# Optimization experiments

Measured on AMD Instinct MI355X. Metric: run time of the kernel, lower is better.

The kernel has to match this reference:

```python
import jax, jax.numpy as jnp
import numpy as np

EPS = 1e-12

def _layer_norm(x, g, b):
    mu = jnp.mean(x, axis=-1, keepdims=True)
    var = jnp.mean(jnp.square(x - mu), axis=-1, keepdims=True)
    return (x - mu) * jax.lax.rsqrt(var + EPS) * g + b

def setup_inputs() -> dict:
    key = jax.random.key(0)
    ks = jax.random.split(key, 16)
    B, S, D, H, F = 2, 2048, 1024, 16, 4096
    s = 0.02
    inp = {
        "x": jax.random.normal(ks[0], (B, S, D), jnp.float32),
        "Wq": jax.random.normal(ks[1], (D, D), jnp.float32) * s,
        "bq": jnp.zeros((D,), jnp.float32),
        "Wk": jax.random.normal(ks[2], (D, D), jnp.float32) * s,
        "bk": jnp.zeros((D,), jnp.float32),
        "Wv": jax.random.normal(ks[3], (D, D), jnp.float32) * s,
        "bv": jnp.zeros((D,), jnp.float32),
        "Wo": jax.random.normal(ks[4], (D, D), jnp.float32) * s,
        "bo": jnp.zeros((D,), jnp.float32),
        "ln1_g": jnp.ones((D,), jnp.float32),
        "ln1_b": jnp.zeros((D,), jnp.float32),
        "W1": jax.random.normal(ks[5], (D, F), jnp.float32) * s,
        "b1": jnp.zeros((F,), jnp.float32),
        "W2": jax.random.normal(ks[6], (F, D), jnp.float32) * s,
        "b2": jnp.zeros((D,), jnp.float32),
        "ln2_g": jnp.ones((D,), jnp.float32),
        "ln2_b": jnp.zeros((D,), jnp.float32),
    }
    return inp

def reference(x, Wq, bq, Wk, bk, Wv, bv, Wo, bo, ln1_g, ln1_b, W1, b1, W2, b2, ln2_g, ln2_b):
    B, S, D = x.shape
    H = 16
    hd = D // H
    # q/k/v projections -> (B, H, S, hd)
    def split_heads(t):
        return t.reshape(B, S, H, hd).transpose(0, 2, 1, 3)
    q = split_heads(x @ Wq + bq)
    k = split_heads(x @ Wk + bk)
    v = split_heads(x @ Wv + bv)
    # naive attention: QK^T / sqrt(hd), softmax, AV
    scores = jnp.einsum("bhqd,bhkd->bhqk", q, k) / jnp.sqrt(jnp.float32(hd))
    attn = jax.nn.softmax(scores, axis=-1)
    ctx = jnp.einsum("bhqk,bhkd->bhqd", attn, v)
    ctx = ctx.transpose(0, 2, 1, 3).reshape(B, S, D)
    attn_out = _layer_norm(ctx @ Wo + bo, ln1_g, ln1_b)
    # FFN: relu -> gelu (exact, matching torch default) -> fc2 + residual -> LN
    h = jax.nn.gelu(jax.nn.relu(attn_out @ W1 + b1), approximate=False)
    out = _layer_norm(h @ W2 + b2 + attn_out, ln2_g, ln2_b)
    return out
```

## Files before the change

### kernel.cpp

```cpp
#include <hip/hip_runtime.h>
#include <hip/hip_bf16.h>
#include <cstdint>
#include <cstddef>

typedef __attribute__((ext_vector_type(8))) short short8;
typedef __attribute__((ext_vector_type(4))) float f32x4;

#define GLL(gp, lp) __builtin_amdgcn_global_load_lds(                         \
    (const __attribute__((address_space(1))) void*)(gp),                      \
    (__attribute__((address_space(3))) void*)(lp), 16, 0, 0)

static __device__ __forceinline__ unsigned short f2bf(float f) {
    union { float f; uint32_t u; } v; v.f = f;
    uint32_t r = v.u + 0x7FFF + ((v.u >> 16) & 1);
    return (unsigned short)(r >> 16);
}

__global__ void cvt_x_kernel(const float* __restrict__ src,
                             unsigned short* __restrict__ dst, int n4) {
    int i = blockIdx.x * blockDim.x + threadIdx.x;
    if (i < n4) {
        float4 v = *reinterpret_cast<const float4*>(src + (size_t)i * 4);
        unsigned short* d = dst + (size_t)i * 4;
        d[0] = f2bf(v.x); d[1] = f2bf(v.y); d[2] = f2bf(v.z); d[3] = f2bf(v.w);
    }
}

__global__ void tr_all_kernel(
    const float* __restrict__ Wq, const float* __restrict__ Wk,
    const float* __restrict__ Wv, const float* __restrict__ Wo,
    const float* __restrict__ W1, const float* __restrict__ W2,
    unsigned short* __restrict__ WqkvT, unsigned short* __restrict__ WoT,
    unsigned short* __restrict__ W1T, unsigned short* __restrict__ W2T)
{
    __shared__ float tile[32][33];
    const int bid = blockIdx.x;
    const float* src; unsigned short* dst; int K, N, local;
    if (bid < 4096) {
        int seg = bid >> 10; local = bid & 1023; K = 1024; N = 1024;
        src = (seg == 0) ? Wq : (seg == 1) ? Wk : (seg == 2) ? Wv : Wo;
        dst = (seg < 3) ? WqkvT + (size_t)seg * 1024 * 1024 : WoT;
    } else if (bid < 8192) {
        local = bid - 4096; K = 1024; N = 4096; src = W1; dst = W1T;
    } else {
        local = bid - 8192; K = 4096; N = 1024; src = W2; dst = W2T;
    }
    const int ntx = N >> 5;
    const int n0 = (local % ntx) * 32, k0 = (local / ntx) * 32;
    const int tx = threadIdx.x, ty = threadIdx.y;
#pragma unroll
    for (int j = 0; j < 32; j += 8)
        tile[ty + j][tx] = src[(size_t)(k0 + ty + j) * N + n0 + tx];
    __syncthreads();
#pragma unroll
    for (int j = 0; j < 32; j += 8)
        dst[(size_t)(n0 + ty + j) * K + k0 + tx] = f2bf(tile[tx][ty + j]);
}

template <int EPI>
__global__ __launch_bounds__(256) void gemm128_kernel(
    const unsigned short* __restrict__ A, const unsigned short* __restrict__ BT,
    int M, int N, int ld, int Kslice,
    const float* __restrict__ bias0, const float* __restrict__ bias1,
    const float* __restrict__ bias2,
    void* __restrict__ out0, void* __restrict__ out1, void* __restrict__ out2)
{
    __shared__ unsigned short Asm[2][128 * 64];
    __shared__ unsigned short Bsm[2][128 * 64];

    const int t = threadIdx.x;
    const int lane = t & 63, wv = t >> 6;
    const int wr = wv >> 1, wc = wv & 1;

    const int gx = gridDim.x;
    const int nwg = gx * gridDim.y;
    const int id = blockIdx.y * gx + blockIdx.x;
    const int swz = (id & 7) * (nwg >> 3) + (id >> 3);
    const int rowBase = (swz / gx) * 128;
    const int colBase = (swz % gx) * 128;
    const int koff = blockIdx.z * Kslice;

    const int r0 = t >> 3, c0 = t & 7;
    const int cg = c0 ^ (r0 & 7);
    const unsigned short* gA = A + (size_t)(rowBase + r0) * ld + koff + cg * 8;
    const unsigned short* gB = BT + (size_t)(colBase + r0) * ld + koff + cg * 8;

    auto stage = [&](int buf, int kt) {
#pragma unroll
        for (int j = 0; j < 4; j++) {
            GLL(gA + (size_t)(32 * j) * ld + kt, &Asm[buf][t * 8 + 2048 * j]);
            GLL(gB + (size_t)(32 * j) * ld + kt, &Bsm[buf][t * 8 + 2048 * j]);
        }
    };

    int aoff[4][2], boff[4][2];
#pragma unroll
    for (int m = 0; m < 4; m++)
#pragma unroll
        for (int ks = 0; ks < 2; ks++) {
            int rl = wr * 64 + m * 16 + (lane & 15);
            aoff[m][ks] = rl * 64 + (((ks * 4 + (lane >> 4)) ^ (rl & 7)) << 3);
            int cl = wc * 64 + m * 16 + (lane & 15);
            boff[m][ks] = cl * 64 + (((ks * 4 + (lane >> 4)) ^ (cl & 7)) << 3);
        }

    f32x4 acc[4][4];
#pragma unroll
    for (int m = 0; m < 4; m++)
#pragma unroll
        for (int n = 0; n < 4; n++) acc[m][n] = (f32x4){0.f, 0.f, 0.f, 0.f};

    stage(0, 0);
    asm volatile("s_waitcnt vmcnt(0)" ::: "memory");
    __builtin_amdgcn_s_barrier();

    const int nt = Kslice >> 6;
    for (int tt = 0; tt < nt; ++tt) {
        const int cur = tt & 1;
        if (tt + 1 < nt) stage(cur ^ 1, (tt + 1) << 6);

        short8 b[4][2];
#pragma unroll
        for (int n = 0; n < 4; n++)
#pragma unroll
            for (int ks = 0; ks < 2; ks++)
                b[n][ks] = *(const short8*)&Bsm[cur][boff[n][ks]];
        __builtin_amdgcn_s_setprio(1);
#pragma unroll
        for (int m = 0; m < 4; m++) {
            short8 a0 = *(const short8*)&Asm[cur][aoff[m][0]];
            short8 a1 = *(const short8*)&Asm[cur][aoff[m][1]];
#pragma unroll
            for (int n = 0; n < 4; n++) {
                acc[m][n] = __builtin_amdgcn_mfma_f32_16x16x32_bf16(
                    a0, b[n][0], acc[m][n], 0, 0, 0);
                acc[m][n] = __builtin_amdgcn_mfma_f32_16x16x32_bf16(
                    a1, b[n][1], acc[m][n], 0, 0, 0);
            }
        }
        __builtin_amdgcn_s_setprio(0);

        asm volatile("s_waitcnt vmcnt(0)" ::: "memory");
        __builtin_amdgcn_sched_barrier(0);
        __builtin_amdgcn_s_barrier();
    }

#pragma unroll
    for (int m = 0; m < 4; m++) {
#pragma unroll
        for (int n = 0; n < 4; n++) {
            const int col = colBase + wc * 64 + n * 16 + (lane & 15);
#pragma unroll
            for (int i = 0; i < 4; i++) {
                const int row = rowBase + wr * 64 + m * 16 + (lane >> 4) * 4 + i;
                float v = acc[m][n][i];
                if (EPI == 0) {
                    const int bb = row >> 11, s = row & 2047;
                    if (col < 1024) {
                        float q = (v + bias0[col]) * 0.18033688011112042f;
                        int h = col >> 6, d = col & 63;
                        ((unsigned short*)out0)[((size_t)(bb * 16 + h) * 2048 + s) * 64 + d] = f2bf(q);
                    } else if (col < 2048) {
                        int cc = col - 1024;
                        float kv = v + bias1[cc];
                        int h = cc >> 6, d = cc & 63;
                        ((unsigned short*)out1)[((size_t)(bb * 16 + h) * 2048 + s) * 64 + d] = f2bf(kv);
                    } else {
                        int cc = col - 2048;
                        float vv = v + bias2[cc];
                        int h = cc >> 6, d = cc & 63;
                        ((unsigned short*)out2)[((size_t)(bb * 16 + h) * 64 + d) * 2048 + s] = f2bf(vv);
                    }
                } else {
                    ((float*)out0)[(size_t)blockIdx.z * M * N + (size_t)row * N + col] = v;
                }
            }
        }
    }
}

template <int EPI>
__global__ __launch_bounds__(512, 2) void gemm256_kernel(
    const unsigned short* __restrict__ A, const unsigned short* __restrict__ BT,
    int M, int N, int K,
    const float* __restrict__ bias0, void* __restrict__ out0)
{
    extern __shared__ unsigned short lds[];

    const int t = threadIdx.x, lane = t & 63, w = t >> 6;
    const int wm = w >> 2, wn = w & 3;

    const int gx = gridDim.x;
    const int nwg = gx * gridDim.y;
    const int id = blockIdx.y * gx + blockIdx.x;
    const int swz = (id & 7) * (nwg >> 3) + (id >> 3);
    const int rowBase = (swz / gx) * 256;
    const int colBase = (swz % gx) * 256;

    const int r0 = t >> 3, c0 = t & 7;
    const int cg = c0 ^ (r0 & 7);
    const unsigned short* gA = A + (size_t)(rowBase + r0) * K + cg * 8;
    const unsigned short* gB = BT + (size_t)(colBase + r0) * K + cg * 8;

    auto stage = [&](int buf, int kt) {
#pragma unroll
        for (int j = 0; j < 4; j++) {
            GLL(gA + (size_t)(64 * j) * K + kt, &lds[buf * 16384 + t * 8 + 4096 * j]);
            GLL(gB + (size_t)(64 * j) * K + kt, &lds[32768 + buf * 16384 + t * 8 + 4096 * j]);
        }
    };

    int aoff[8][2], boff[4][2];
#pragma unroll
    for (int mf = 0; mf < 8; mf++)
#pragma unroll
        for (int ks = 0; ks < 2; ks++) {
            int rl = wm * 128 + mf * 16 + (lane & 15);
            aoff[mf][ks] = rl * 64 + (((ks * 4 + (lane >> 4)) ^ (rl & 7)) << 3);
        }
#pragma unroll
    for (int nf = 0; nf < 4; nf++)
#pragma unroll
        for (int ks = 0; ks < 2; ks++) {
            int cl = wn * 64 + nf * 16 + (lane & 15);
            boff[nf][ks] = cl * 64 + (((ks * 4 + (lane >> 4)) ^ (cl & 7)) << 3);
        }

    f32x4 acc[8][4];
#pragma unroll
    for (int mf = 0; mf < 8; mf++)
#pragma unroll
        for (int nf = 0; nf < 4; nf++) acc[mf][nf] = (f32x4){0.f, 0.f, 0.f, 0.f};

    stage(0, 0);
    asm volatile("s_waitcnt vmcnt(0)" ::: "memory");
    __builtin_amdgcn_s_barrier();

    const int nt = K >> 6;
    for (int tt = 0; tt < nt; ++tt) {
        const int cur = tt & 1;
        const int ab = cur * 16384, bbase = 32768 + cur * 16384;
        if (tt + 1 < nt) stage(cur ^ 1, (tt + 1) << 6);

        short8 b[4][2];
#pragma unroll
        for (int nf = 0; nf < 4; nf++)
#pragma unroll
            for (int ks = 0; ks < 2; ks++)
                b[nf][ks] = *(const short8*)&lds[bbase + boff[nf][ks]];
        __builtin_amdgcn_s_setprio(1);
#pragma unroll
        for (int mf = 0; mf < 8; mf++) {
            short8 a0 = *(const short8*)&lds[ab + aoff[mf][0]];
            short8 a1 = *(const short8*)&lds[ab + aoff[mf][1]];
#pragma unroll
            for (int nf = 0; nf < 4; nf++) {
                acc[mf][nf] = __builtin_amdgcn_mfma_f32_16x16x32_bf16(
                    a0, b[nf][0], acc[mf][nf], 0, 0, 0);
                acc[mf][nf] = __builtin_amdgcn_mfma_f32_16x16x32_bf16(
                    a1, b[nf][1], acc[mf][nf], 0, 0, 0);
            }
        }
        __builtin_amdgcn_s_setprio(0);

        asm volatile("s_waitcnt vmcnt(0)" ::: "memory");
        __builtin_amdgcn_sched_barrier(0);
        __builtin_amdgcn_s_barrier();
    }

#pragma unroll
    for (int mf = 0; mf < 8; mf++) {
#pragma unroll
        for (int nf = 0; nf < 4; nf++) {
            const int col = colBase + wn * 64 + nf * 16 + (lane & 15);
#pragma unroll
            for (int i = 0; i < 4; i++) {
                const int row = rowBase + wm * 128 + mf * 16 + (lane >> 4) * 4 + i;
                float z = acc[mf][nf][i] + bias0[col];
                if (z > 0.f) {
                    float u = 0.7978845608f * (z + 0.044715f * z * z * z);
                    float e = __builtin_amdgcn_exp2f(u * 2.8853900817779268f);
                    z = z * (1.f - 1.f / (e + 1.f));
                } else z = 0.f;
                ((unsigned short*)out0)[(size_t)row * N + col] = f2bf(z);
            }
        }
    }
}

__global__ __launch_bounds__(256, 4) void flash_attn_kernel(
    const unsigned short* __restrict__ Qb, const unsigned short* __restrict__ Kb,
    const unsigned short* __restrict__ VT, unsigned short* __restrict__ ctxb)
{
    __shared__ unsigned short Ksm[2][64 * 64];
    __shared__ unsigned short Vsm[2][64 * 64];
    __shared__ unsigned short Psm[4][16 * 64];

    const int bh = blockIdx.y;
    const int q0 = blockIdx.x * 64;
    const int t = threadIdx.x, lane = t & 63, wv = t >> 6;

    const unsigned short* Qg = Qb + (size_t)bh * 2048 * 64;
    const unsigned short* Kg = Kb + (size_t)bh * 2048 * 64;
    const unsigned short* Vg = VT + (size_t)bh * 64 * 2048;

    short8 qf[2];
    {
        int r = q0 + wv * 16 + (lane & 15);
        qf[0] = *(const short8*)&Qg[(size_t)r * 64 + ((lane >> 4) << 3)];
        qf[1] = *(const short8*)&Qg[(size_t)r * 64 + 32 + ((lane >> 4) << 3)];
    }

    short8 onesf;
#pragma unroll
    for (int j = 0; j < 8; j++) onesf[j] = (short)0x3F80;

    f32x4 o[4], lacc;
#pragma unroll
    for (int n = 0; n < 4; n++) o[n] = (f32x4){0.f, 0.f, 0.f, 0.f};
    lacc = (f32x4){0.f, 0.f, 0.f, 0.f};

    const int r0 = t >> 3, sl = t & 7;
    const int cg0 = sl ^ (r0 & 7);
    const int r1 = (256 + t) >> 3;
    const int cg1 = sl ^ (r1 & 7);

    auto stageKV = [&](int buf, int kt) {
        GLL(&Kg[(size_t)(kt + r0) * 64 + cg0 * 8], &Ksm[buf][t * 8]);
        GLL(&Kg[(size_t)(kt + r1) * 64 + cg1 * 8], &Ksm[buf][(256 + t) * 8]);
        GLL(&Vg[(size_t)r0 * 2048 + kt + cg0 * 8], &Vsm[buf][t * 8]);
        GLL(&Vg[(size_t)r1 * 2048 + kt + cg1 * 8], &Vsm[buf][(256 + t) * 8]);
    };

    unsigned short* P = &Psm[wv][0];

    int pwaddr[4][4];
#pragma unroll
    for (int n = 0; n < 4; n++)
#pragma unroll
        for (int i = 0; i < 4; i++) {
            int rl = (lane >> 4) * 4 + i;
            int col = n * 16 + (lane & 15);
            pwaddr[n][i] = rl * 64 + ((((col >> 3) ^ (rl & 7)) << 3) | (col & 7));
        }

    stageKV(0, 0);
    asm volatile("s_waitcnt vmcnt(0)" ::: "memory");
    __builtin_amdgcn_s_barrier();

    for (int tt = 0; tt < 32; ++tt) {
        const int cur = tt & 1;
        if (tt + 1 < 32) stageKV(cur ^ 1, (tt + 1) << 6);

        f32x4 s[4];
        __builtin_amdgcn_s_setprio(1);
#pragma unroll
        for (int n = 0; n < 4; n++) {
            s[n] = (f32x4){0.f, 0.f, 0.f, 0.f};
            int rl = n * 16 + (lane & 15);
#pragma unroll
            for (int kb = 0; kb < 2; kb++) {
                int slot = ((kb << 2) + (lane >> 4)) ^ (rl & 7);
                short8 kf = *(const short8*)&Ksm[cur][rl * 64 + slot * 8];
                s[n] = __builtin_amdgcn_mfma_f32_16x16x32_bf16(qf[kb], kf, s[n], 0, 0, 0);
            }
        }
        __builtin_amdgcn_s_setprio(0);

#pragma unroll
        for (int n = 0; n < 4; n++)
#pragma unroll
            for (int i = 0; i < 4; i++) {
                float p = __builtin_amdgcn_exp2f(s[n][i]);
                union { float f; uint32_t u; } pv; pv.f = p;
                P[pwaddr[n][i]] = (unsigned short)(pv.u >> 16);
            }

        short8 pf[2];
        {
            int rl = lane & 15;
#pragma unroll
            for (int kb = 0; kb < 2; kb++) {
                int slot = ((kb << 2) + (lane >> 4)) ^ (rl & 7);
                pf[kb] = *(const short8*)&P[rl * 64 + slot * 8];
            }
        }
        __builtin_amdgcn_s_setprio(1);
        lacc = __builtin_amdgcn_mfma_f32_16x16x32_bf16(pf[0], onesf, lacc, 0, 0, 0);
        lacc = __builtin_amdgcn_mfma_f32_16x16x32_bf16(pf[1], onesf, lacc, 0, 0, 0);
#pragma unroll
        for (int n = 0; n < 4; n++) {
            int d = n * 16 + (lane & 15);
#pragma unroll
            for (int kb = 0; kb < 2; kb++) {
                int slot = ((kb << 2) + (lane >> 4)) ^ (d & 7);
                short8 vf = *(const short8*)&Vsm[cur][d * 64 + slot * 8];
                o[n] = __builtin_amdgcn_mfma_f32_16x16x32_bf16(pf[kb], vf, o[n], 0, 0, 0);
            }
        }
        __builtin_amdgcn_s_setprio(0);

        asm volatile("s_waitcnt vmcnt(0)" ::: "memory");
        __builtin_amdgcn_sched_barrier(0);
        __builtin_amdgcn_s_barrier();
    }

    const int bb = bh >> 4, h = bh & 15;
#pragma unroll
    for (int i = 0; i < 4; i++) {
        float linv = 1.f / lacc[i];
        int srow = q0 + wv * 16 + (lane >> 4) * 4 + i;
#pragma unroll
        for (int n = 0; n < 4; n++) {
            int d = n * 16 + (lane & 15);
            ctxb[((size_t)(bb * 2048 + srow)) * 1024 + h * 64 + d] =
                f2bf(o[n][i] * linv);
        }
    }
}

__global__ __launch_bounds__(256) void ln_kernel(
    const float* __restrict__ in0, const float* __restrict__ in1,
    const float* __restrict__ resid, const float* __restrict__ bias,
    const float* __restrict__ g, const float* __restrict__ bta,
    float* __restrict__ outf, unsigned short* __restrict__ outb)
{
    const int row = blockIdx.x;
    const int t = threadIdx.x, lane = t & 63, wv = t >> 6;
    const size_t base = (size_t)row * 1024 + t * 4;

    float4 xv = *reinterpret_cast<const float4*>(in0 + base);
    if (in1) {
        float4 v1 = *reinterpret_cast<const float4*>(in1 + base);
        xv.x += v1.x; xv.y += v1.y; xv.z += v1.z; xv.w += v1.w;
    }
    if (resid) {
        float4 rv = *reinterpret_cast<const float4*>(resid + base);
        xv.x += rv.x; xv.y += rv.y; xv.z += rv.z; xv.w += rv.w;
    }
    {
        float4 bv = *reinterpret_cast<const float4*>(bias + t * 4);
        xv.x += bv.x; xv.y += bv.y; xv.z += bv.z; xv.w += bv.w;
    }

    float s = xv.x + xv.y + xv.z + xv.w;
    float ss = xv.x * xv.x + xv.y * xv.y + xv.z * xv.z + xv.w * xv.w;
#pragma unroll
    for (int off = 1; off < 64; off <<= 1) {
        s += __shfl_xor(s, off);
        ss += __shfl_xor(ss, off);
    }
    __shared__ float red[8];
    if (lane == 0) { red[wv] = s; red[4 + wv] = ss; }
    __syncthreads();
    s = red[0] + red[1] + red[2] + red[3];
    ss = red[4] + red[5] + red[6] + red[7];
    const float mu = s * (1.f / 1024.f);
    const float var = ss * (1.f / 1024.f) - mu * mu;
    const float inv = rsqrtf(var + 1e-12f);

    float4 gv = *reinterpret_cast<const float4*>(g + t * 4);
    float4 bv = *reinterpret_cast<const float4*>(bta + t * 4);
    float o0 = (xv.x - mu) * inv * gv.x + bv.x;
    float o1 = (xv.y - mu) * inv * gv.y + bv.y;
    float o2 = (xv.z - mu) * inv * gv.z + bv.z;
    float o3 = (xv.w - mu) * inv * gv.w + bv.w;

    *reinterpret_cast<float4*>(outf + base) = (float4){o0, o1, o2, o3};
    if (outb) {
        unsigned short* ob = outb + base;
        ob[0] = f2bf(o0); ob[1] = f2bf(o1); ob[2] = f2bf(o2); ob[3] = f2bf(o3);
    }
}

extern "C" void kernel_launch(void* const* d_in, const int* in_sizes, int n_in,
                              void* d_out, int out_size, void* d_ws, size_t ws_size,
                              hipStream_t stream) {
    const float* x     = (const float*)d_in[0];
    const float* Wq    = (const float*)d_in[1];
    const float* bq    = (const float*)d_in[2];
    const float* Wk    = (const float*)d_in[3];
    const float* bk    = (const float*)d_in[4];
    const float* Wv    = (const float*)d_in[5];
    const float* bv    = (const float*)d_in[6];
    const float* Wo    = (const float*)d_in[7];
    const float* bo    = (const float*)d_in[8];
    const float* ln1_g = (const float*)d_in[9];
    const float* ln1_b = (const float*)d_in[10];
    const float* W1    = (const float*)d_in[11];
    const float* b1    = (const float*)d_in[12];
    const float* W2    = (const float*)d_in[13];
    const float* b2    = (const float*)d_in[14];
    const float* ln2_g = (const float*)d_in[15];
    const float* ln2_b = (const float*)d_in[16];
    float* out = (float*)d_out;

    const int B = 2, S = 2048, D = 1024, H = 16, F = 4096;
    const int M = B * S;

    char* w = (char*)d_ws;
    size_t off = 0;
    auto alloc = [&](size_t bytes) {
        size_t o = off; off += (bytes + 255) & ~(size_t)255; return o;
    };
    unsigned short* xb      = (unsigned short*)(w + alloc((size_t)M * D * 2));
    unsigned short* WqkvT   = (unsigned short*)(w + alloc((size_t)3 * D * D * 2));
    unsigned short* WoT     = (unsigned short*)(w + alloc((size_t)D * D * 2));
    unsigned short* W1T     = (unsigned short*)(w + alloc((size_t)D * F * 2));
    unsigned short* W2T     = (unsigned short*)(w + alloc((size_t)F * D * 2));
    unsigned short* Qbuf    = (unsigned short*)(w + alloc((size_t)M * D * 2));
    unsigned short* Kbuf    = (unsigned short*)(w + alloc((size_t)M * D * 2));
    unsigned short* VTbuf   = (unsigned short*)(w + alloc((size_t)M * D * 2));
    float*          z0      = (float*)(w + alloc((size_t)M * D * 4));
    float*          z1      = (float*)(w + alloc((size_t)M * D * 4));
    float*          attnlnf = (float*)(w + alloc((size_t)M * D * 4));
    unsigned short* attnlnb = (unsigned short*)(w + alloc((size_t)M * D * 2));
    unsigned short* hbuf    = (unsigned short*)(w + alloc((size_t)M * F * 2));
    unsigned short* ctxb    = xb;

    hipFuncSetAttribute((const void*)gemm256_kernel<2>,
                        hipFuncAttributeMaxDynamicSharedMemorySize, 131072);

    cvt_x_kernel<<<(M * D / 4 + 255) / 256, 256, 0, stream>>>(x, xb, M * D / 4);
    tr_all_kernel<<<12288, dim3(32, 8), 0, stream>>>(
        Wq, Wk, Wv, Wo, W1, W2, WqkvT, WoT, W1T, W2T);

    gemm128_kernel<0><<<dim3(3 * D / 128, M / 128, 1), 256, 0, stream>>>(
        xb, WqkvT, M, 3 * D, D, D, bq, bk, bv, Qbuf, Kbuf, VTbuf);

    flash_attn_kernel<<<dim3(S / 64, B * H), 256, 0, stream>>>(
        Qbuf, Kbuf, VTbuf, ctxb);

    gemm128_kernel<4><<<dim3(D / 128, M / 128, 2), 256, 0, stream>>>(
        ctxb, WoT, M, D, D, D / 2, nullptr, nullptr, nullptr, z0, nullptr, nullptr);

    ln_kernel<<<M, 256, 0, stream>>>(z0, z1, nullptr, bo, ln1_g, ln1_b,
                                     attnlnf, attnlnb);

    gemm256_kernel<2><<<dim3(F / 256, M / 256), 512, 131072, stream>>>(
        attnlnb, W1T, M, F, D, b1, hbuf);

    gemm128_kernel<4><<<dim3(D / 128, M / 128, 2), 256, 0, stream>>>(
        hbuf, W2T, M, D, F, F / 2, nullptr, nullptr, nullptr, z0, nullptr, nullptr);

    ln_kernel<<<M, 256, 0, stream>>>(z0, z1, attnlnf, b2, ln2_g, ln2_b,
                                     out, nullptr);
}
```

Before: 257.2 us.

## Store split-K partials and residual in bf16, merge input cast into transpose kernel

The split-K GEMM outputs z0/z1 are now stored as bf16 instead of fp32. The LN kernels read them as bf16, and the residual path reuses the bf16 LN1 output instead of a separate fp32 copy. This halves the write and read traffic between the projection GEMMs and the layer norms, and drops one fp32 buffer write. The x-to-bf16 conversion is folded into the weight transpose kernel to save a launch. The cost is lower precision, because the partial sums and the residual are each rounded to bf16 before the sum.

Result: faster. 246.9 us (-4.0%).

```diff
diff --git a/kernel.cpp b/kernel.cpp
--- a/kernel.cpp
+++ b/kernel.cpp
@@ -5,6 +5,7 @@
 
 typedef __attribute__((ext_vector_type(8))) short short8;
 typedef __attribute__((ext_vector_type(4))) float f32x4;
+typedef __attribute__((ext_vector_type(4))) unsigned short ushort4v;
 
 #define GLL(gp, lp) __builtin_amdgcn_global_load_lds(                         \
     (const __attribute__((address_space(1))) void*)(gp),                      \
@@ -15,26 +16,32 @@
     uint32_t r = v.u + 0x7FFF + ((v.u >> 16) & 1);
     return (unsigned short)(r >> 16);
 }
-
-__global__ void cvt_x_kernel(const float* __restrict__ src,
-                             unsigned short* __restrict__ dst, int n4) {
-    int i = blockIdx.x * blockDim.x + threadIdx.x;
-    if (i < n4) {
-        float4 v = *reinterpret_cast<const float4*>(src + (size_t)i * 4);
-        unsigned short* d = dst + (size_t)i * 4;
-        d[0] = f2bf(v.x); d[1] = f2bf(v.y); d[2] = f2bf(v.z); d[3] = f2bf(v.w);
-    }
-}
-
-__global__ void tr_all_kernel(
+static __device__ __forceinline__ float bf2f(unsigned short u) {
+    union { uint32_t u; float f; } v; v.u = (uint32_t)u << 16; return v.f;
+}
+
+__global__ void pre_all_kernel(
+    const float* __restrict__ x,
     const float* __restrict__ Wq, const float* __restrict__ Wk,
     const float* __restrict__ Wv, const float* __restrict__ Wo,
     const float* __restrict__ W1, const float* __restrict__ W2,
+    unsigned short* __restrict__ xb,
     unsigned short* __restrict__ WqkvT, unsigned short* __restrict__ WoT,
     unsigned short* __restrict__ W1T, unsigned short* __restrict__ W2T)
 {
+    const int bid = blockIdx.x;
+    const int tx = threadIdx.x, ty = threadIdx.y;
+    if (bid >= 12288) {
+        const int tid = ty * 32 + tx;
+        const size_t base = (size_t)(bid - 12288) * 2048 + tid * 8;
+        float4 v0 = *reinterpret_cast<const float4*>(x + base);
+        float4 v1 = *reinterpret_cast<const float4*>(x + base + 4);
+        unsigned short* d = xb + base;
+        d[0] = f2bf(v0.x); d[1] = f2bf(v0.y); d[2] = f2bf(v0.z); d[3] = f2bf(v0.w);
+        d[4] = f2bf(v1.x); d[5] = f2bf(v1.y); d[6] = f2bf(v1.z); d[7] = f2bf(v1.w);
+        return;
+    }
     __shared__ float tile[32][33];
-    const int bid = blockIdx.x;
     const float* src; unsigned short* dst; int K, N, local;
     if (bid < 4096) {
         int seg = bid >> 10; local = bid & 1023; K = 1024; N = 1024;
@@ -47,7 +54,6 @@
     }
     const int ntx = N >> 5;
     const int n0 = (local % ntx) * 32, k0 = (local / ntx) * 32;
-    const int tx = threadIdx.x, ty = threadIdx.y;
 #pragma unroll
     for (int j = 0; j < 32; j += 8)
         tile[ty + j][tx] = src[(size_t)(k0 + ty + j) * N + n0 + tx];
@@ -172,7 +178,8 @@
                         ((unsigned short*)out2)[((size_t)(bb * 16 + h) * 64 + d) * 2048 + s] = f2bf(vv);
                     }
                 } else {
-                    ((float*)out0)[(size_t)blockIdx.z * M * N + (size_t)row * N + col] = v;
+                    ((unsigned short*)out0)[(size_t)blockIdx.z * M * N + (size_t)row * N + col]
+                        = f2bf(v);
                 }
             }
         }
@@ -420,8 +427,8 @@
 }
 
 __global__ __launch_bounds__(256) void ln_kernel(
-    const float* __restrict__ in0, const float* __restrict__ in1,
-    const float* __restrict__ resid, const float* __restrict__ bias,
+    const unsigned short* __restrict__ in0, const unsigned short* __restrict__ in1,
+    const unsigned short* __restrict__ resid, const float* __restrict__ bias,
     const float* __restrict__ g, const float* __restrict__ bta,
     float* __restrict__ outf, unsigned short* __restrict__ outb)
 {
@@ -429,14 +436,17 @@
     const int t = threadIdx.x, lane = t & 63, wv = t >> 6;
     const size_t base = (size_t)row * 1024 + t * 4;
 
-    float4 xv = *reinterpret_cast<const float4*>(in0 + base);
-    if (in1) {
-        float4 v1 = *reinterpret_cast<const float4*>(in1 + base);
-        xv.x += v1.x; xv.y += v1.y; xv.z += v1.z; xv.w += v1.w;
-    }
+    ushort4v u0 = *reinterpret_cast<const ushort4v*>(in0 + base);
+    ushort4v u1 = *reinterpret_cast<const ushort4v*>(in1 + base);
+    float4 xv;
+    xv.x = bf2f(u0[0]) + bf2f(u1[0]);
+    xv.y = bf2f(u0[1]) + bf2f(u1[1]);
+    xv.z = bf2f(u0[2]) + bf2f(u1[2]);
+    xv.w = bf2f(u0[3]) + bf2f(u1[3]);
     if (resid) {
-        float4 rv = *reinterpret_cast<const float4*>(resid + base);
-        xv.x += rv.x; xv.y += rv.y; xv.z += rv.z; xv.w += rv.w;
+        ushort4v ur = *reinterpret_cast<const ushort4v*>(resid + base);
+        xv.x += bf2f(ur[0]); xv.y += bf2f(ur[1]);
+        xv.z += bf2f(ur[2]); xv.w += bf2f(ur[3]);
     }
     {
         float4 bv = *reinterpret_cast<const float4*>(bias + t * 4);
@@ -466,7 +476,8 @@
     float o2 = (xv.z - mu) * inv * gv.z + bv.z;
     float o3 = (xv.w - mu) * inv * gv.w + bv.w;
 
-    *reinterpret_cast<float4*>(outf + base) = (float4){o0, o1, o2, o3};
+    if (outf)
+        *reinterpret_cast<float4*>(outf + base) = (float4){o0, o1, o2, o3};
     if (outb) {
         unsigned short* ob = outb + base;
         ob[0] = f2bf(o0); ob[1] = f2bf(o1); ob[2] = f2bf(o2); ob[3] = f2bf(o3);
@@ -511,9 +522,8 @@
     unsigned short* Qbuf    = (unsigned short*)(w + alloc((size_t)M * D * 2));
     unsigned short* Kbuf    = (unsigned short*)(w + alloc((size_t)M * D * 2));
     unsigned short* VTbuf   = (unsigned short*)(w + alloc((size_t)M * D * 2));
-    float*          z0      = (float*)(w + alloc((size_t)M * D * 4));
-    float*          z1      = (float*)(w + alloc((size_t)M * D * 4));
-    float*          attnlnf = (float*)(w + alloc((size_t)M * D * 4));
+    unsigned short* z0      = (unsigned short*)(w + alloc((size_t)M * D * 2));
+    unsigned short* z1      = (unsigned short*)(w + alloc((size_t)M * D * 2));
     unsigned short* attnlnb = (unsigned short*)(w + alloc((size_t)M * D * 2));
     unsigned short* hbuf    = (unsigned short*)(w + alloc((size_t)M * F * 2));
     unsigned short* ctxb    = xb;
@@ -521,9 +531,8 @@
     hipFuncSetAttribute((const void*)gemm256_kernel<2>,
                         hipFuncAttributeMaxDynamicSharedMemorySize, 131072);
 
-    cvt_x_kernel<<<(M * D / 4 + 255) / 256, 256, 0, stream>>>(x, xb, M * D / 4);
-    tr_all_kernel<<<12288, dim3(32, 8), 0, stream>>>(
-        Wq, Wk, Wv, Wo, W1, W2, WqkvT, WoT, W1T, W2T);
+    pre_all_kernel<<<14336, dim3(32, 8), 0, stream>>>(
+        x, Wq, Wk, Wv, Wo, W1, W2, xb, WqkvT, WoT, W1T, W2T);
 
     gemm128_kernel<0><<<dim3(3 * D / 128, M / 128, 1), 256, 0, stream>>>(
         xb, WqkvT, M, 3 * D, D, D, bq, bk, bv, Qbuf, Kbuf, VTbuf);
@@ -535,7 +544,7 @@
         ctxb, WoT, M, D, D, D / 2, nullptr, nullptr, nullptr, z0, nullptr, nullptr);
 
     ln_kernel<<<M, 256, 0, stream>>>(z0, z1, nullptr, bo, ln1_g, ln1_b,
-                                     attnlnf, attnlnb);
+                                     nullptr, attnlnb);
 
     gemm256_kernel<2><<<dim3(F / 256, M / 256), 512, 131072, stream>>>(
         attnlnb, W1T, M, F, D, b1, hbuf);
@@ -543,6 +552,6 @@
     gemm128_kernel<4><<<dim3(D / 128, M / 128, 2), 256, 0, stream>>>(
         hbuf, W2T, M, D, F, F / 2, nullptr, nullptr, nullptr, z0, nullptr, nullptr);
 
-    ln_kernel<<<M, 256, 0, stream>>>(z0, z1, attnlnf, b2, ln2_g, ln2_b,
+    ln_kernel<<<M, 256, 0, stream>>>(z0, z1, attnlnb, b2, ln2_g, ln2_b,
                                      out, nullptr);
 }
```
